# Optimization experiments

Hardware: AMD Instinct MI355X
Metric: run time of the kernel (lower is better)

The kernel has to match this reference:

```python
import jax, jax.numpy as jnp
import numpy as np

EPS = 1e-5  # torch LayerNorm default


def _ln(x, w, b):
    m = jnp.mean(x, axis=-1, keepdims=True)
    v = jnp.mean((x - m) ** 2, axis=-1, keepdims=True)
    return (x - m) / jnp.sqrt(v + EPS) * w + b


def _conv1x1(x, w, b):
    # x: [B,C,H,W], w: [O,C], b: [O]
    return jnp.einsum('bchw,oc->bohw', x, w) + b[None, :, None, None]


def setup_inputs() -> dict:
    key = jax.random.key(0)
    ks = jax.random.split(key, 5)
    B, Cin, H, W = 8, 384, 64, 64
    D, N = 128, 512
    s = lambda k, shape, scale=0.02: jax.random.normal(k, shape, jnp.float32) * scale
    return {
        'x': jax.random.normal(ks[0], (B, Cin, H, W), jnp.float32),
        'DR': jax.random.normal(ks[1], (N, D), jnp.float32),
        'conv_in_w': s(ks[2], (D, Cin)),
        'conv_in_b': jnp.zeros((D,), jnp.float32),
        'sem_w': s(ks[3], (D, D)),
        'sem_b': jnp.zeros((D,), jnp.float32),
        'norm1_w': jnp.ones((D,), jnp.float32),
        'norm1_b': jnp.zeros((D,), jnp.float32),
        'norm2_w': jnp.ones((D,), jnp.float32),
        'norm2_b': jnp.zeros((D,), jnp.float32),
        'conv_out_w': s(ks[4], (Cin, D)),
        'conv_out_b': jnp.zeros((Cin,), jnp.float32),
    }


def reference(x, DR, conv_in_w, conv_in_b, sem_w, sem_b, norm1_w, norm1_b,
              norm2_w, norm2_b, conv_out_w, conv_out_b):
    B, _, H, W = x.shape
    N = DR.shape[0]
    x_align = _conv1x1(x, conv_in_w, conv_in_b)                      # [B,D,H,W]
    x_sem = _conv1x1(x_align, sem_w, sem_b)                          # semantic_extra (1x1 conv)
    x_sem = x_sem.transpose(0, 2, 3, 1).reshape(B, H * W, -1)        # [B,HW,D]
    x_sem = _ln(x_sem, norm1_w, norm1_b)
    dr = _ln(DR, norm2_w, norm2_b).T                                 # [D,N] (same for all batches)
    # NOTE: original applies norm_1 TWICE for the numerator (faithful quirk)
    c_u = jnp.einsum('bld,dn->bln', _ln(x_sem, norm1_w, norm1_b), dr)  # [B,HW,N]
    c_d_l = jnp.sqrt(jnp.sum(x_sem ** 2, axis=-1, keepdims=True))      # [B,HW,1]
    c_d_r = jnp.sqrt(jnp.sum(dr ** 2, axis=0, keepdims=True))[None]    # [1,1,N]
    sim = c_u / (c_d_l * c_d_r)
    sim_soft = jax.nn.softmax(sim, axis=-1)                          # [B,HW,N]
    sim2d = sim_soft.transpose(0, 2, 1).reshape(B, N, H, W)
    degrad = jnp.einsum('bln,dn->bdl', sim_soft, dr).reshape(B, -1, H, W)  # [B,D,H,W]
    # pow-mask with per-batch min-max normalization
    mask_v = jnp.max(sim2d ** 3, axis=1, keepdims=True)              # [B,1,H,W]
    mn = jnp.min(mask_v.reshape(B, -1), axis=1).reshape(B, 1, 1, 1)
    mx = jnp.max(mask_v.reshape(B, -1), axis=1).reshape(B, 1, 1, 1)
    mask_v = 1.0 - (mask_v - mn) / (mx - mn)
    # topk row selection (torch fancy indexing gives [B,B,K,N]; squeeze(1) is a no-op for B>1)
    max_values = jnp.max(sim_soft, axis=2)                           # [B,HW]
    K = (H * W) // 50
    _, top_idx = jax.lax.top_k(max_values, K)                        # [B,K]
    results = jnp.take(sim_soft, top_idx, axis=1)                    # [B,B,K,N]
    out_img = _conv1x1(degrad, conv_out_w, conv_out_b)               # [B,Cin,H,W]
    return (mask_v, out_img, results)
```

## Files before the change

### kernel.cpp

```cpp
#include <hip/hip_runtime.h>
#include <cstdint>

#define EPS 1e-5f
#define BB   8
#define CIN  384
#define HWs  4096
#define LT   32768
#define DD   128
#define NN   512
#define TOPK 81
#define PSTR 528

typedef short short8 __attribute__((ext_vector_type(8)));
typedef float f32x4  __attribute__((ext_vector_type(4)));

__device__ __forceinline__ unsigned short f2bf(float x) {
  unsigned u = __float_as_uint(x);
  u += 0x7fffu + ((u >> 16) & 1u);
  return (unsigned short)(u >> 16);
}
__device__ __forceinline__ float bf2f(unsigned u16) {
  return __uint_as_float(u16 << 16);
}
__device__ __forceinline__ void put_frag(unsigned short* buf, int tile, int rc, int k, float v) {
  int ks = k >> 5, g = (k >> 3) & 3, j = k & 7;
  int basehw = ((tile * 4 + ks) * 2) * 512 + (g * 16 + rc) * 8 + j;
  unsigned short hi = f2bf(v);
  buf[basehw] = hi;
  buf[basehw + 512] = f2bf(v - bf2f(hi));
}

__device__ __forceinline__ void dr_body(int n, int lane, const float* __restrict__ DR,
    const float* __restrict__ w2, const float* __restrict__ b2,
    const float* __restrict__ w1, const float* __restrict__ b1,
    unsigned short* __restrict__ drwF, unsigned short* __restrict__ drlnF,
    float* __restrict__ t2, float* __restrict__ rcr) {
  const float* row = DR + n * DD;
  float x0 = row[lane], x1 = row[lane + 64];
  float s = x0 + x1, sq = x0 * x0 + x1 * x1;
  #pragma unroll
  for (int o = 32; o; o >>= 1) { s += __shfl_xor(s, o); sq += __shfl_xor(sq, o); }
  float m = s * (1.f / 128.f);
  float v = sq * (1.f / 128.f) - m * m;
  float inv = rsqrtf(v + EPS);
  float y0 = (x0 - m) * inv * w2[lane] + b2[lane];
  float y1 = (x1 - m) * inv * w2[lane + 64] + b2[lane + 64];
  int nt = n >> 4, cc = n & 15;
  put_frag(drwF, nt, cc, lane, y0 * w1[lane]);
  put_frag(drwF, nt, cc, lane + 64, y1 * w1[lane + 64]);
  int ks = n >> 5, gB = (n >> 3) & 3, j = n & 7;
  {
    int d = lane;
    unsigned short hi = f2bf(y0);
    int base = (((d >> 4) * 16 + ks) * 2) * 512 + (gB * 16 + (d & 15)) * 8 + j;
    drlnF[base] = hi;
    drlnF[base + 512] = f2bf(y0 - bf2f(hi));
  }
  {
    int d = lane + 64;
    unsigned short hi = f2bf(y1);
    int base = (((d >> 4) * 16 + ks) * 2) * 512 + (gB * 16 + (d & 15)) * 8 + j;
    drlnF[base] = hi;
    drlnF[base + 512] = f2bf(y1 - bf2f(hi));
  }
  float pt2 = y0 * b1[lane] + y1 * b1[lane + 64];
  float pss = y0 * y0 + y1 * y1;
  #pragma unroll
  for (int o = 32; o; o >>= 1) { pt2 += __shfl_xor(pt2, o); pss += __shfl_xor(pss, o); }
  if (lane == 0) { t2[n] = pt2; rcr[n] = rsqrtf(pss); }
}

__device__ __forceinline__ void bprep_body(const float* __restrict__ src,
    unsigned short* __restrict__ dst, int K, int rt, int kb, int t) {
  int m = t >> 4, kg = t & 15;
  int k0 = kb * 128 + kg * 8;
  const float* s = src + (size_t)(rt * 16 + m) * K + k0;
  float4 f0 = *(const float4*)s;
  float4 f1 = *(const float4*)(s + 4);
  float vs[8] = {f0.x, f0.y, f0.z, f0.w, f1.x, f1.y, f1.z, f1.w};
  short8 hi, lo;
  #pragma unroll
  for (int j = 0; j < 8; ++j) {
    unsigned short h = f2bf(vs[j]);
    hi[j] = (short)h;
    lo[j] = (short)f2bf(vs[j] - bf2f(h));
  }
  int nkt = K >> 5;
  int ks = k0 >> 5, g = (k0 >> 3) & 3;
  short8* D8 = (short8*)dst;
  int base = ((rt * nkt + ks) * 2) * 64 + g * 16 + m;
  D8[base] = hi;
  D8[base + 64] = lo;
}

__global__ __launch_bounds__(256) void k_prep(const float* __restrict__ DR,
    const float* __restrict__ n2w, const float* __restrict__ n2b,
    const float* __restrict__ n1w, const float* __restrict__ n1b,
    unsigned short* __restrict__ drwF, unsigned short* __restrict__ drlnF,
    float* __restrict__ t2, float* __restrict__ rcr,
    const float* __restrict__ win, unsigned short* __restrict__ WinF,
    const float* __restrict__ sw, unsigned short* __restrict__ semWF,
    const float* __restrict__ wout, unsigned short* __restrict__ WoF) {
  int blk = blockIdx.x, t = threadIdx.x;
  if (blk < 128) {
    dr_body(blk * 4 + (t >> 6), t & 63, DR, n2w, n2b, n1w, n1b, drwF, drlnF, t2, rcr);
  } else if (blk < 152) {
    int idx = blk - 128;
    bprep_body(win, WinF, CIN, idx & 7, idx >> 3, t);
  } else if (blk < 160) {
    bprep_body(sw, semWF, DD, blk - 152, 0, t);
  } else {
    bprep_body(wout, WoF, DD, blk - 160, 0, t);
  }
}

__global__ __launch_bounds__(256, 3) void k_convsem(const float* __restrict__ x,
    const unsigned short* __restrict__ WinF, const float* __restrict__ bin,
    const unsigned short* __restrict__ semWF, const float* __restrict__ sb,
    const float* __restrict__ w1, const float* __restrict__ b1,
    unsigned short* __restrict__ ApF, float* __restrict__ rclv) {
  __shared__ float xt[CIN * 33];
  __shared__ float sredS[32][4], sredQ[32][4];
  __shared__ float rowM[32], rowI[32];
  int t = threadIdx.x;
  int w = t >> 6, lane = t & 63, m = lane & 15, g = lane >> 4;
  int l0 = blockIdx.x * 32;
  int b = l0 >> 12, hw0 = l0 & 4095;
  {
    const float* xs = x + (size_t)b * CIN * HWs + (size_t)(t >> 3) * HWs + hw0 + (t & 7) * 4;
    float4 v[12];
    #pragma unroll
    for (int r = 0; r < 12; ++r)
      v[r] = *(const float4*)(xs + (size_t)(r * 32) * HWs);
    #pragma unroll
    for (int r = 0; r < 12; ++r) {
      float* d = &xt[(r * 32 + (t >> 3)) * 33 + (t & 7) * 4];
      d[0] = v[r].x; d[1] = v[r].y; d[2] = v[r].z; d[3] = v[r].w;
    }
  }
  __syncthreads();
  const short8* B8 = (const short8*)WinF;
  f32x4 acc[2][2];
  #pragma unroll
  for (int lt = 0; lt < 2; ++lt)
    #pragma unroll
    for (int j2 = 0; j2 < 2; ++j2) acc[lt][j2] = (f32x4){0.f, 0.f, 0.f, 0.f};
  for (int ks = 0; ks < 12; ++ks) {
    short8 ah[2], al[2];
    #pragma unroll
    for (int lt = 0; lt < 2; ++lt) {
      #pragma unroll
      for (int j = 0; j < 8; ++j) {
        float xv = xt[(ks * 32 + g * 8 + j) * 33 + lt * 16 + m];
        unsigned short h = f2bf(xv);
        ah[lt][j] = (short)h;
        al[lt][j] = (short)f2bf(xv - bf2f(h));
      }
    }
    #pragma unroll
    for (int j2 = 0; j2 < 2; ++j2) {
      int dt = w * 2 + j2;
      short8 bh = B8[((dt * 12 + ks) * 2 + 0) * 64 + lane];
      short8 bl = B8[((dt * 12 + ks) * 2 + 1) * 64 + lane];
      #pragma unroll
      for (int lt = 0; lt < 2; ++lt) {
        acc[lt][j2] = __builtin_amdgcn_mfma_f32_16x16x32_bf16(ah[lt], bh, acc[lt][j2], 0, 0, 0);
        acc[lt][j2] = __builtin_amdgcn_mfma_f32_16x16x32_bf16(ah[lt], bl, acc[lt][j2], 0, 0, 0);
        acc[lt][j2] = __builtin_amdgcn_mfma_f32_16x16x32_bf16(al[lt], bh, acc[lt][j2], 0, 0, 0);
      }
    }
  }
  __syncthreads();
  unsigned int* plane = (unsigned int*)xt;
  {
    float bia[2] = {bin[w * 32 + m], bin[w * 32 + 16 + m]};
    #pragma unroll
    for (int lt = 0; lt < 2; ++lt)
      #pragma unroll
      for (int j2 = 0; j2 < 2; ++j2)
        #pragma unroll
        for (int r = 0; r < 4; ++r) {
          float v = acc[lt][j2][r] + bia[j2];
          unsigned short h = f2bf(v);
          unsigned short lo = f2bf(v - bf2f(h));
          plane[(lt * 16 + g * 4 + r) * 132 + (w * 2 + j2) * 16 + m] =
              (unsigned)h | ((unsigned)lo << 16);
        }
  }
  __syncthreads();
  const short8* S8 = (const short8*)semWF;
  f32x4 acc2[2][2];
  #pragma unroll
  for (int lt = 0; lt < 2; ++lt)
    #pragma unroll
    for (int j2 = 0; j2 < 2; ++j2) acc2[lt][j2] = (f32x4){0.f, 0.f, 0.f, 0.f};
  #pragma unroll
  for (int ks2 = 0; ks2 < 4; ++ks2) {
    short8 ah2[2], al2[2];
    #pragma unroll
    for (int lt = 0; lt < 2; ++lt) {
      const unsigned* src = &plane[(lt * 16 + m) * 132 + ks2 * 32 + g * 8];
      uint4 p0 = *(const uint4*)(src);
      uint4 p1 = *(const uint4*)(src + 4);
      unsigned uu[8] = {p0.x, p0.y, p0.z, p0.w, p1.x, p1.y, p1.z, p1.w};
      unsigned* ahp = (unsigned*)&ah2[lt];
      unsigned* alp = (unsigned*)&al2[lt];
      #pragma unroll
      for (int jj = 0; jj < 4; ++jj) {
        unsigned e0 = uu[2 * jj], e1 = uu[2 * jj + 1];
        ahp[jj] = (e0 & 0xffffu) | (e1 << 16);
        alp[jj] = (e0 >> 16) | (e1 & 0xffff0000u);
      }
    }
    #pragma unroll
    for (int j2 = 0; j2 < 2; ++j2) {
      int dt = w * 2 + j2;
      short8 bh = S8[((dt * 4 + ks2) * 2 + 0) * 64 + lane];
      short8 bl = S8[((dt * 4 + ks2) * 2 + 1) * 64 + lane];
      #pragma unroll
      for (int lt = 0; lt < 2; ++lt) {
        acc2[lt][j2] = __builtin_amdgcn_mfma_f32_16x16x32_bf16(ah2[lt], bh, acc2[lt][j2], 0, 0, 0);
        acc2[lt][j2] = __builtin_amdgcn_mfma_f32_16x16x32_bf16(ah2[lt], bl, acc2[lt][j2], 0, 0, 0);
        acc2[lt][j2] = __builtin_amdgcn_mfma_f32_16x16x32_bf16(al2[lt], bh, acc2[lt][j2], 0, 0, 0);
      }
    }
  }
  {
    float bia2[2] = {sb[w * 32 + m], sb[w * 32 + 16 + m]};
    #pragma unroll
    for (int lt = 0; lt < 2; ++lt)
      #pragma unroll
      for (int j2 = 0; j2 < 2; ++j2)
        #pragma unroll
        for (int r = 0; r < 4; ++r) acc2[lt][j2][r] += bia2[j2];
  }
  float s1[2][4], q1[2][4];
  #pragma unroll
  for (int lt = 0; lt < 2; ++lt)
    #pragma unroll
    for (int r = 0; r < 4; ++r) {
      float a = acc2[lt][0][r], b2v = acc2[lt][1][r];
      s1[lt][r] = a + b2v;
      q1[lt][r] = a * a + b2v * b2v;
    }
  #pragma unroll
  for (int o = 1; o < 16; o <<= 1)
    #pragma unroll
    for (int lt = 0; lt < 2; ++lt)
      #pragma unroll
      for (int r = 0; r < 4; ++r) {
        s1[lt][r] += __shfl_xor(s1[lt][r], o);
        q1[lt][r] += __shfl_xor(q1[lt][r], o);
      }
  if (m == 0) {
    #pragma unroll
    for (int lt = 0; lt < 2; ++lt)
      #pragma unroll
      for (int r = 0; r < 4; ++r) {
        sredS[lt * 16 + g * 4 + r][w] = s1[lt][r];
        sredQ[lt * 16 + g * 4 + r][w] = q1[lt][r];
      }
  }
  __syncthreads();
  if (t < 32) {
    float S = sredS[t][0] + sredS[t][1] + sredS[t][2] + sredS[t][3];
    float Q = sredQ[t][0] + sredQ[t][1] + sredQ[t][2] + sredQ[t][3];
    float mu = S * (1.f / 128.f);
    float var = Q * (1.f / 128.f) - mu * mu;
    rowM[t] = mu;
    rowI[t] = rsqrtf(var + EPS);
  }
  __syncthreads();
  float w1v[2] = {w1[w * 32 + m], w1[w * 32 + 16 + m]};
  float b1v[2] = {b1[w * 32 + m], b1[w * 32 + 16 + m]};
  #pragma unroll
  for (int lt = 0; lt < 2; ++lt)
    #pragma unroll
    for (int r = 0; r < 4; ++r) {
      float mu = rowM[lt * 16 + g * 4 + r];
      float iv = rowI[lt * 16 + g * 4 + r];
      float y0 = (acc2[lt][0][r] - mu) * iv * w1v[0] + b1v[0];
      float y1 = (acc2[lt][1][r] - mu) * iv * w1v[1] + b1v[1];
      acc2[lt][0][r] = y0; acc2[lt][1][r] = y1;
      s1[lt][r] = y0 + y1;
      q1[lt][r] = y0 * y0 + y1 * y1;
    }
  #pragma unroll
  for (int o = 1; o < 16; o <<= 1)
    #pragma unroll
    for (int lt = 0; lt < 2; ++lt)
      #pragma unroll
      for (int r = 0; r < 4; ++r) {
        s1[lt][r] += __shfl_xor(s1[lt][r], o);
        q1[lt][r] += __shfl_xor(q1[lt][r], o);
      }
  if (m == 0) {
    #pragma unroll
    for (int lt = 0; lt < 2; ++lt)
      #pragma unroll
      for (int r = 0; r < 4; ++r) {
        sredS[lt * 16 + g * 4 + r][w] = s1[lt][r];
        sredQ[lt * 16 + g * 4 + r][w] = q1[lt][r];
      }
  }
  __syncthreads();
  if (t < 32) {
    float S = sredS[t][0] + sredS[t][1] + sredS[t][2] + sredS[t][3];
    float Q = sredQ[t][0] + sredQ[t][1] + sredQ[t][2] + sredQ[t][3];
    float m2 = S * (1.f / 128.f);
    float v2 = Q * (1.f / 128.f) - m2 * m2;
    float inv2 = rsqrtf(v2 + EPS);
    float rcl = rsqrtf(Q);
    rowM[t] = m2;
    rowI[t] = inv2 * rcl;
    rclv[l0 + t] = rcl;
  }
  __syncthreads();
  float* planef = (float*)xt;
  #pragma unroll
  for (int lt = 0; lt < 2; ++lt)
    #pragma unroll
    for (int r = 0; r < 4; ++r) {
      float m2 = rowM[lt * 16 + g * 4 + r];
      float sc = rowI[lt * 16 + g * 4 + r];
      planef[(lt * 16 + g * 4 + r) * 132 + w * 32 + m] = (acc2[lt][0][r] - m2) * sc;
      planef[(lt * 16 + g * 4 + r) * 132 + w * 32 + 16 + m] = (acc2[lt][1][r] - m2) * sc;
    }
  __syncthreads();
  short8* O8 = (short8*)ApF;
  #pragma unroll
  for (int it = 0; it < 2; ++it) {
    int idx = it * 256 + t;
    int l = idx & 31, dq = idx >> 5;
    const float* src = &planef[l * 132 + dq * 8];
    float4 f0 = *(const float4*)src;
    float4 f1 = *(const float4*)(src + 4);
    float vs[8] = {f0.x, f0.y, f0.z, f0.w, f1.x, f1.y, f1.z, f1.w};
    short8 hi, lo;
    #pragma unroll
    for (int j = 0; j < 8; ++j) {
      unsigned short h = f2bf(vs[j]);
      hi[j] = (short)h;
      lo[j] = (short)f2bf(vs[j] - bf2f(h));
    }
    int ltg = (l0 + l) >> 4;
    int idx8 = ((ltg * 4 + (dq >> 2)) * 2) * 64 + (dq & 3) * 16 + (l & 15);
    O8[idx8] = hi;
    O8[idx8 + 64] = lo;
  }
}

__global__ __launch_bounds__(256, 4) void k_sdeg(const unsigned short* __restrict__ ApF,
    const unsigned short* __restrict__ drwF, const float* __restrict__ t2g,
    const float* __restrict__ rcrg, const float* __restrict__ rclg,
    const unsigned short* __restrict__ drlnF, const unsigned short* __restrict__ WoF,
    const float* __restrict__ bo,
    unsigned short* __restrict__ pF, float* __restrict__ maxv,
    float* __restrict__ out_img) {
  __shared__ __align__(16) float sredM[32][4];
  __shared__ __align__(16) float sredS[32][4];
  __shared__ __align__(16) unsigned short plds[32 * PSTR];
  int t = threadIdx.x;
  int w = t >> 6, lane = t & 63, c = lane & 15, g = lane >> 4;
  int l0 = blockIdx.x * 32;
  int lt0 = blockIdx.x * 2;
  const short8* A8 = (const short8*)ApF;
  const short8* B8 = (const short8*)drwF;
  f32x4 acc[2][8];
  #pragma unroll
  for (int il = 0; il < 2; ++il)
    #pragma unroll
    for (int jn = 0; jn < 8; ++jn) acc[il][jn] = (f32x4){0.f, 0.f, 0.f, 0.f};
  #pragma unroll
  for (int ks = 0; ks < 4; ++ks) {
    short8 ah0 = A8[((lt0 * 4 + ks) * 2 + 0) * 64 + lane];
    short8 al0 = A8[((lt0 * 4 + ks) * 2 + 1) * 64 + lane];
    short8 ah1 = A8[(((lt0 + 1) * 4 + ks) * 2 + 0) * 64 + lane];
    short8 al1 = A8[(((lt0 + 1) * 4 + ks) * 2 + 1) * 64 + lane];
    #pragma unroll
    for (int jn = 0; jn < 8; ++jn) {
      int nt = w * 8 + jn;
      short8 bh = B8[((nt * 4 + ks) * 2 + 0) * 64 + lane];
      short8 bl = B8[((nt * 4 + ks) * 2 + 1) * 64 + lane];
      acc[0][jn] = __builtin_amdgcn_mfma_f32_16x16x32_bf16(ah0, bh, acc[0][jn], 0, 0, 0);
      acc[0][jn] = __builtin_amdgcn_mfma_f32_16x16x32_bf16(ah0, bl, acc[0][jn], 0, 0, 0);
      acc[0][jn] = __builtin_amdgcn_mfma_f32_16x16x32_bf16(al0, bh, acc[0][jn], 0, 0, 0);
      acc[1][jn] = __builtin_amdgcn_mfma_f32_16x16x32_bf16(ah1, bh, acc[1][jn], 0, 0, 0);
      acc[1][jn] = __builtin_amdgcn_mfma_f32_16x16x32_bf16(ah1, bl, acc[1][jn], 0, 0, 0);
      acc[1][jn] = __builtin_amdgcn_mfma_f32_16x16x32_bf16(al1, bh, acc[1][jn], 0, 0, 0);
    }
  }
  float rcrv[8], t2v[8];
  #pragma unroll
  for (int jn = 0; jn < 8; ++jn) {
    int n = w * 128 + jn * 16 + c;
    rcrv[jn] = rcrg[n]; t2v[jn] = t2g[n];
  }
  float rclr[2][4];
  #pragma unroll
  for (int il = 0; il < 2; ++il)
    #pragma unroll
    for (int r = 0; r < 4; ++r)
      rclr[il][r] = rclg[l0 + il * 16 + g * 4 + r];
  float M[2][4];
  #pragma unroll
  for (int il = 0; il < 2; ++il)
    #pragma unroll
    for (int r = 0; r < 4; ++r) M[il][r] = -1e30f;
  #pragma unroll
  for (int il = 0; il < 2; ++il)
    #pragma unroll
    for (int jn = 0; jn < 8; ++jn) {
      f32x4 a = acc[il][jn];
      #pragma unroll
      for (int r = 0; r < 4; ++r) {
        float s = rcrv[jn] * (a[r] + rclr[il][r] * t2v[jn]);
        a[r] = s;
        M[il][r] = fmaxf(M[il][r], s);
      }
      acc[il][jn] = a;
    }
  #pragma unroll
  for (int o = 1; o < 16; o <<= 1)
    #pragma unroll
    for (int il = 0; il < 2; ++il)
      #pragma unroll
      for (int r = 0; r < 4; ++r)
        M[il][r] = fmaxf(M[il][r], __shfl_xor(M[il][r], o));
  if (c == 0) {
    #pragma unroll
    for (int il = 0; il < 2; ++il)
      #pragma unroll
      for (int r = 0; r < 4; ++r)
        sredM[il * 16 + g * 4 + r][w] = M[il][r];
  }
  __syncthreads();
  float Mf[2][4];
  #pragma unroll
  for (int il = 0; il < 2; ++il)
    #pragma unroll
    for (int r = 0; r < 4; ++r) {
      f32x4 mv = *(const f32x4*)(&sredM[il * 16 + g * 4 + r][0]);
      Mf[il][r] = fmaxf(fmaxf(mv[0], mv[1]), fmaxf(mv[2], mv[3]));
    }
  float S[2][4];
  #pragma unroll
  for (int il = 0; il < 2; ++il)
    #pragma unroll
    for (int r = 0; r < 4; ++r) S[il][r] = 0.f;
  #pragma unroll
  for (int il = 0; il < 2; ++il)
    #pragma unroll
    for (int jn = 0; jn < 8; ++jn) {
      f32x4 a = acc[il][jn];
      #pragma unroll
      for (int r = 0; r < 4; ++r) {
        float e = __expf(a[r] - Mf[il][r]);
        a[r] = e;
        S[il][r] += e;
      }
      acc[il][jn] = a;
    }
  #pragma unroll
  for (int o = 1; o < 16; o <<= 1)
    #pragma unroll
    for (int il = 0; il < 2; ++il)
      #pragma unroll
      for (int r = 0; r < 4; ++r)
        S[il][r] += __shfl_xor(S[il][r], o);
  if (c == 0) {
    #pragma unroll
    for (int il = 0; il < 2; ++il)
      #pragma unroll
      for (int r = 0; r < 4; ++r)
        sredS[il * 16 + g * 4 + r][w] = S[il][r];
  }
  __syncthreads();
  float RS[2][4];
  #pragma unroll
  for (int il = 0; il < 2; ++il)
    #pragma unroll
    for (int r = 0; r < 4; ++r) {
      f32x4 sv = *(const f32x4*)(&sredS[il * 16 + g * 4 + r][0]);
      float tot = sv[0] + sv[1] + sv[2] + sv[3];
      RS[il][r] = 1.f / tot;
    }
  if (w == 0 && c == 0) {
    #pragma unroll
    for (int il = 0; il < 2; ++il)
      #pragma unroll
      for (int r = 0; r < 4; ++r)
        maxv[l0 + il * 16 + g * 4 + r] = RS[il][r];
  }
  #pragma unroll
  for (int il = 0; il < 2; ++il)
    #pragma unroll
    for (int jn = 0; jn < 8; ++jn)
      #pragma unroll
      for (int r = 0; r < 4; ++r)
        plds[(il * 16 + g * 4 + r) * PSTR + w * 128 + jn * 16 + c] =
            f2bf(acc[il][jn][r] * RS[il][r]);
  __syncthreads();
  const short8* D8 = (const short8*)drlnF;
  f32x4 accd[2][2];
  #pragma unroll
  for (int lt = 0; lt < 2; ++lt)
    #pragma unroll
    for (int j2 = 0; j2 < 2; ++j2) accd[lt][j2] = (f32x4){0.f, 0.f, 0.f, 0.f};
  for (int ks = 0; ks < 16; ++ks) {
    const unsigned short* sp = &plds[c * PSTR + ks * 32 + g * 8];
    short8 pa0 = *(const short8*)sp;
    short8 pa1 = *(const short8*)(sp + 16 * PSTR);
    #pragma unroll
    for (int j2 = 0; j2 < 2; ++j2) {
      int dt = w * 2 + j2;
      short8 bh = D8[((dt * 16 + ks) * 2 + 0) * 64 + lane];
      short8 bl = D8[((dt * 16 + ks) * 2 + 1) * 64 + lane];
      accd[0][j2] = __builtin_amdgcn_mfma_f32_16x16x32_bf16(pa0, bh, accd[0][j2], 0, 0, 0);
      accd[0][j2] = __builtin_amdgcn_mfma_f32_16x16x32_bf16(pa0, bl, accd[0][j2], 0, 0, 0);
      accd[1][j2] = __builtin_amdgcn_mfma_f32_16x16x32_bf16(pa1, bh, accd[1][j2], 0, 0, 0);
      accd[1][j2] = __builtin_amdgcn_mfma_f32_16x16x32_bf16(pa1, bl, accd[1][j2], 0, 0, 0);
    }
  }
  short8* P8o = (short8*)pF;
  #pragma unroll
  for (int it = 0; it < 8; ++it) {
    int slot = it * 256 + t;
    int ltl = slot >> 10;
    int ks = (slot >> 6) & 15;
    int gB = (slot >> 4) & 3;
    int mrow = slot & 15;
    int row = ltl * 16 + mrow;
    int n0 = ks * 32 + gB * 8;
    short8 v = *(const short8*)(&plds[row * PSTR + n0]);
    __builtin_nontemporal_store(v, &P8o[blockIdx.x * 2048 + slot]);
  }
  __syncthreads();
  float* smem2 = (float*)plds;
  #pragma unroll
  for (int lt = 0; lt < 2; ++lt)
    #pragma unroll
    for (int j2 = 0; j2 < 2; ++j2)
      #pragma unroll
      for (int r = 0; r < 4; ++r)
        smem2[(lt * 16 + g * 4 + r) * 132 + w * 32 + j2 * 16 + c] = accd[lt][j2][r];
  __syncthreads();
  const short8* W8 = (const short8*)WoF;
  f32x4 acco[2][6];
  #pragma unroll
  for (int lt = 0; lt < 2; ++lt)
    #pragma unroll
    for (int ot = 0; ot < 6; ++ot) acco[lt][ot] = (f32x4){0.f, 0.f, 0.f, 0.f};
  #pragma unroll
  for (int ks2 = 0; ks2 < 4; ++ks2) {
    short8 dh[2];
    #pragma unroll
    for (int lt = 0; lt < 2; ++lt) {
      const float* src = &smem2[(lt * 16 + c) * 132 + ks2 * 32 + g * 8];
      float4 f0 = *(const float4*)src;
      float4 f1 = *(const float4*)(src + 4);
      float vs[8] = {f0.x, f0.y, f0.z, f0.w, f1.x, f1.y, f1.z, f1.w};
      #pragma unroll
      for (int j = 0; j < 8; ++j) dh[lt][j] = (short)f2bf(vs[j]);
    }
    #pragma unroll
    for (int ot = 0; ot < 6; ++ot) {
      int otg = w * 6 + ot;
      short8 wh = W8[((otg * 4 + ks2) * 2 + 0) * 64 + lane];
      short8 wl = W8[((otg * 4 + ks2) * 2 + 1) * 64 + lane];
      #pragma unroll
      for (int lt = 0; lt < 2; ++lt) {
        acco[lt][ot] = __builtin_amdgcn_mfma_f32_16x16x32_bf16(dh[lt], wh, acco[lt][ot], 0, 0, 0);
        acco[lt][ot] = __builtin_amdgcn_mfma_f32_16x16x32_bf16(dh[lt], wl, acco[lt][ot], 0, 0, 0);
      }
    }
  }
  int b = l0 >> 12, hw0 = l0 & 4095;
  float* ob = out_img + (size_t)b * CIN * HWs + hw0;
  #pragma unroll
  for (int ot = 0; ot < 6; ++ot) {
    float bov = bo[w * 96 + ot * 16 + c];
    #pragma unroll
    for (int lt = 0; lt < 2; ++lt) {
      f32x4 vv = acco[lt][ot];
      f32x4 o4 = {vv[0] + bov, vv[1] + bov, vv[2] + bov, vv[3] + bov};
      __builtin_nontemporal_store(o4,
          (f32x4*)(ob + (size_t)(w * 96 + ot * 16 + c) * HWs + lt * 16 + g * 4));
    }
  }
}

__global__ __launch_bounds__(256) void k_topk(const float* __restrict__ maxv,
                                              int* __restrict__ tix,
                                              float* __restrict__ outm) {
  __shared__ unsigned int hist[4][256];
  __shared__ unsigned long long slist[TOPK];
  __shared__ unsigned long long bc_prefix;
  __shared__ int bc_need, scount;
  __shared__ float smn[4], smx[4];
  int b = blockIdx.x, t = threadIdx.x;
  int w = t >> 6;
  unsigned long long key[16];
  #pragma unroll
  for (int j = 0; j < 16; ++j) {
    int idx = t + j * 256;
    unsigned int bits = __float_as_uint(maxv[b * HWs + idx]);
    key[j] = ((unsigned long long)bits << 12) | (unsigned)(4095 - idx);
  }
  {
    float c3[16];
    float mn = 1e30f, mx = -1e30f;
    #pragma unroll
    for (int j = 0; j < 16; ++j) {
      float x = __uint_as_float((unsigned)(key[j] >> 12));
      float cc = x * x * x;
      c3[j] = cc;
      mn = fminf(mn, cc); mx = fmaxf(mx, cc);
    }
    #pragma unroll
    for (int o = 32; o; o >>= 1) { mn = fminf(mn, __shfl_xor(mn, o)); mx = fmaxf(mx, __shfl_xor(mx, o)); }
    if ((t & 63) == 0) { smn[w] = mn; smx[w] = mx; }
    __syncthreads();
    mn = fminf(fminf(smn[0], smn[1]), fminf(smn[2], smn[3]));
    mx = fmaxf(fmaxf(smx[0], smx[1]), fmaxf(smx[2], smx[3]));
    float sc = 1.f / (mx - mn);
    #pragma unroll
    for (int j = 0; j < 16; ++j)
      outm[b * HWs + t + j * 256] = 1.f - (c3[j] - mn) * sc;
  }
  if (t == 0) { bc_prefix = 0ull; bc_need = TOPK; scount = 0; }
  for (int r = 0; r < 6; ++r) {
    int shift = 40 - 8 * r;
    unsigned int* hflat = (unsigned int*)hist;
    hflat[t] = 0; hflat[t + 256] = 0; hflat[t + 512] = 0; hflat[t + 768] = 0;
    __syncthreads();
    unsigned long long prefix = bc_prefix;
    int bins[16];
    #pragma unroll
    for (int j = 0; j < 16; ++j)
      bins[j] = ((key[j] >> (shift + 8)) == prefix) ? (int)((key[j] >> shift) & 255) : -1;
    #pragma unroll
    for (int j = 0; j < 16; ++j) {
      if (bins[j] >= 0) {
        int cnt = 1;
        #pragma unroll
        for (int j2 = j + 1; j2 < 16; ++j2)
          if (bins[j2] == bins[j]) { bins[j2] = -1; ++cnt; }
        atomicAdd(&hist[w][bins[j]], (unsigned)cnt);
      }
    }
    __syncthreads();
    if (t < 64) {
      int cb[4], s = 0;
      #pragma unroll
      for (int j = 0; j < 4; ++j) {
        int bin = 255 - (t * 4 + j);
        cb[j] = (int)(hist[0][bin] + hist[1][bin] + hist[2][bin] + hist[3][bin]);
        s += cb[j];
      }
      int P = s;
      #pragma unroll
      for (int o = 1; o < 64; o <<= 1) {
        int u = __shfl_up(P, o);
        if (t >= o) P += u;
      }
      int need = bc_need;
      unsigned long long mask = __ballot(P >= need);
      int first = __ffsll((long long)mask) - 1;
      if (t == first) {
        int acc = P - s;
        #pragma unroll
        for (int j = 0; j < 4; ++j) {
          if (acc + cb[j] >= need) {
            bc_prefix = (prefix << 8) | (unsigned)(255 - (t * 4 + j));
            bc_need = need - acc;
            break;
          }
          acc += cb[j];
        }
      }
    }
    __syncthreads();
  }
  unsigned long long K81 = bc_prefix;
  #pragma unroll
  for (int j = 0; j < 16; ++j)
    if (key[j] >= K81) {
      int pos = atomicAdd(&scount, 1);
      slist[pos] = key[j];
    }
  __syncthreads();
  if (t < TOPK) {
    unsigned long long mine = slist[t];
    int rank = 0;
    for (int i = 0; i < TOPK; ++i) rank += (slist[i] > mine) ? 1 : 0;
    tix[b * TOPK + rank] = 4095 - (int)(mine & 0xFFFull);
  }
}

__global__ __launch_bounds__(128) void k_gather(const unsigned short* __restrict__ pF,
    const int* __restrict__ tix, float* __restrict__ outr) {
  int gB_ = blockIdx.x;
  int k = gB_ % TOPK;
  int bb = gB_ / TOPK;
  int b2 = bb & 7, b = bb >> 3;
  int l = b * HWs + tix[b2 * TOPK + k];
  int lt = l >> 4, mrow = l & 15;
  int t = threadIdx.x;
  int ks = t >> 3, gq = (t >> 1) & 3, j0 = (t & 1) * 4;
  int base = ((lt * 16 + ks) * 64 + gq * 16 + mrow) * 8 + j0;
  const unsigned* src = (const unsigned*)(pF + base);
  unsigned u0 = src[0], u1 = src[1];
  f32x4 v = {bf2f(u0 & 0xffffu), bf2f(u0 >> 16), bf2f(u1 & 0xffffu), bf2f(u1 >> 16)};
  __builtin_nontemporal_store(v, (f32x4*)(outr + (size_t)gB_ * NN + t * 4));
}

extern "C" void kernel_launch(void* const* d_in, const int* in_sizes, int n_in,
                              void* d_out, int out_size, void* d_ws, size_t ws_size,
                              hipStream_t stream) {
  const float* x    = (const float*)d_in[0];
  const float* DR   = (const float*)d_in[1];
  const float* win  = (const float*)d_in[2];
  const float* bin  = (const float*)d_in[3];
  const float* sw   = (const float*)d_in[4];
  const float* sb   = (const float*)d_in[5];
  const float* n1w  = (const float*)d_in[6];
  const float* n1b  = (const float*)d_in[7];
  const float* n2w  = (const float*)d_in[8];
  const float* n2b  = (const float*)d_in[9];
  const float* wout = (const float*)d_in[10];
  const float* bout = (const float*)d_in[11];
  float* out = (float*)d_out;
  float* W = (float*)d_ws;

  unsigned short* drwF  = (unsigned short*)(W);
  float* t2   = W + 65536;
  float* rcr  = W + 66048;
  float* rclv = W + 66560;
  float* maxv = W + 99328;
  unsigned short* drlnF = (unsigned short*)(W + 132096);
  unsigned short* WoF   = (unsigned short*)(W + 197632);
  unsigned short* WinF  = (unsigned short*)(W + 246784);
  unsigned short* semWF = (unsigned short*)(W + 295936);
  unsigned short* ApF   = (unsigned short*)(W + 312320);
  unsigned short* pF    = (unsigned short*)(W + 4506624);
  int*   tix  = (int*)(W + 12895232);

  float* out_mask = out;
  float* out_img  = out + 32768;
  float* out_res  = out + 32768 + 12582912;

  k_prep   <<<184, 256, 0, stream>>>(DR, n2w, n2b, n1w, n1b, drwF, drlnF, t2, rcr,
                                     win, WinF, sw, semWF, wout, WoF);
  k_convsem<<<1024, 256, 0, stream>>>(x, WinF, bin, semWF, sb, n1w, n1b, ApF, rclv);
  k_sdeg   <<<1024, 256, 0, stream>>>(ApF, drwF, t2, rcr, rclv, drlnF, WoF, bout,
                                      pF, maxv, out_img);
  k_topk   <<<BB,   256, 0, stream>>>(maxv, tix, out_mask);
  k_gather <<<BB * BB * TOPK, 128, 0, stream>>>(pF, tix, out_res);
}
```

Before: 218.4 us.

## Recompute selected softmax rows in gather instead of materializing full probability matrix

```diff
diff --git a/kernel.cpp b/kernel.cpp
--- a/kernel.cpp
+++ b/kernel.cpp
@@ -355,7 +355,7 @@
     const float* __restrict__ rcrg, const float* __restrict__ rclg,
     const unsigned short* __restrict__ drlnF, const unsigned short* __restrict__ WoF,
     const float* __restrict__ bo,
-    unsigned short* __restrict__ pF, float* __restrict__ maxv,
+    float* __restrict__ mfv, float* __restrict__ maxv,
     float* __restrict__ out_img) {
   __shared__ __align__(16) float sredM[32][4];
   __shared__ __align__(16) float sredS[32][4];
@@ -489,8 +489,10 @@
     #pragma unroll
     for (int il = 0; il < 2; ++il)
       #pragma unroll
-      for (int r = 0; r < 4; ++r)
+      for (int r = 0; r < 4; ++r) {
         maxv[l0 + il * 16 + g * 4 + r] = RS[il][r];
+        mfv[l0 + il * 16 + g * 4 + r] = Mf[il][r];
+      }
   }
   #pragma unroll
   for (int il = 0; il < 2; ++il)
@@ -522,19 +524,6 @@
       accd[1][j2] = __builtin_amdgcn_mfma_f32_16x16x32_bf16(pa1, bl, accd[1][j2], 0, 0, 0);
     }
   }
-  short8* P8o = (short8*)pF;
-  #pragma unroll
-  for (int it = 0; it < 8; ++it) {
-    int slot = it * 256 + t;
-    int ltl = slot >> 10;
-    int ks = (slot >> 6) & 15;
-    int gB = (slot >> 4) & 3;
-    int mrow = slot & 15;
-    int row = ltl * 16 + mrow;
-    int n0 = ks * 32 + gB * 8;
-    short8 v = *(const short8*)(&plds[row * PSTR + n0]);
-    __builtin_nontemporal_store(v, &P8o[blockIdx.x * 2048 + slot]);
-  }
   __syncthreads();
   float* smem2 = (float*)plds;
   #pragma unroll
@@ -583,9 +572,8 @@
     #pragma unroll
     for (int lt = 0; lt < 2; ++lt) {
       f32x4 vv = acco[lt][ot];
-      f32x4 o4 = {vv[0] + bov, vv[1] + bov, vv[2] + bov, vv[3] + bov};
-      __builtin_nontemporal_store(o4,
-          (f32x4*)(ob + (size_t)(w * 96 + ot * 16 + c) * HWs + lt * 16 + g * 4));
+      float4 o4 = {vv[0] + bov, vv[1] + bov, vv[2] + bov, vv[3] + bov};
+      *(float4*)(ob + (size_t)(w * 96 + ot * 16 + c) * HWs + lt * 16 + g * 4) = o4;
     }
   }
 }
@@ -698,21 +686,71 @@
   }
 }
 
-__global__ __launch_bounds__(128) void k_gather(const unsigned short* __restrict__ pF,
+__global__ __launch_bounds__(256) void k_gather(const unsigned short* __restrict__ ApF,
+    const unsigned short* __restrict__ drwF, const float* __restrict__ t2g,
+    const float* __restrict__ rcrg, const float* __restrict__ rclg,
+    const float* __restrict__ mfv, const float* __restrict__ rsv,
     const int* __restrict__ tix, float* __restrict__ outr) {
-  int gB_ = blockIdx.x;
-  int k = gB_ % TOPK;
-  int bb = gB_ / TOPK;
-  int b2 = bb & 7, b = bb >> 3;
-  int l = b * HWs + tix[b2 * TOPK + k];
-  int lt = l >> 4, mrow = l & 15;
+  __shared__ float As[8][128];
+  __shared__ float rclS[8], mfS[8], rsS[8];
+  int blk = blockIdx.x;
+  int k = blk % TOPK, b2 = blk / TOPK;
+  int lloc = tix[b2 * TOPK + k];
   int t = threadIdx.x;
-  int ks = t >> 3, gq = (t >> 1) & 3, j0 = (t & 1) * 4;
-  int base = ((lt * 16 + ks) * 64 + gq * 16 + mrow) * 8 + j0;
-  const unsigned* src = (const unsigned*)(pF + base);
-  unsigned u0 = src[0], u1 = src[1];
-  f32x4 v = {bf2f(u0 & 0xffffu), bf2f(u0 >> 16), bf2f(u1 & 0xffffu), bf2f(u1 >> 16)};
-  __builtin_nontemporal_store(v, (f32x4*)(outr + (size_t)gB_ * NN + t * 4));
+  {
+    int idx = t;
+    #pragma unroll
+    for (int it = 0; it < 4; ++it, idx += 256) {
+      int bb = idx >> 7, d = idx & 127;
+      int grow = bb * HWs + lloc;
+      int ltg = grow >> 4, mrow = grow & 15;
+      int ks = d >> 5, gq = (d >> 3) & 3, j = d & 7;
+      int sbase = (((ltg * 4 + ks) * 2) * 64 + gq * 16 + mrow) * 8 + j;
+      As[bb][d] = bf2f(ApF[sbase]) + bf2f(ApF[sbase + 512]);
+    }
+    if (t < 8) {
+      int grow = t * HWs + lloc;
+      rclS[t] = rclg[grow];
+      mfS[t] = mfv[grow];
+      rsS[t] = rsv[grow];
+    }
+  }
+  __syncthreads();
+  #pragma unroll
+  for (int half = 0; half < 2; ++half) {
+    int n = half * 256 + t;
+    int nt = n >> 4, cc = n & 15;
+    float dot[8];
+    #pragma unroll
+    for (int bb = 0; bb < 8; ++bb) dot[bb] = 0.f;
+    #pragma unroll
+    for (int d8 = 0; d8 < 16; ++d8) {
+      int ks = d8 >> 2, gq = d8 & 3;
+      int sbase = ((nt * 4 + ks) * 2) * 512 + (gq * 16 + cc) * 8;
+      const unsigned* hp = (const unsigned*)(drwF + sbase);
+      const unsigned* lp = (const unsigned*)(drwF + sbase + 512);
+      float bcol[8];
+      #pragma unroll
+      for (int jj = 0; jj < 4; ++jj) {
+        unsigned h2 = hp[jj], l2 = lp[jj];
+        bcol[2 * jj]     = bf2f(h2 & 0xffffu) + bf2f(l2 & 0xffffu);
+        bcol[2 * jj + 1] = bf2f(h2 >> 16)     + bf2f(l2 >> 16);
+      }
+      #pragma unroll
+      for (int bb = 0; bb < 8; ++bb) {
+        #pragma unroll
+        for (int j = 0; j < 8; ++j)
+          dot[bb] += As[bb][d8 * 8 + j] * bcol[j];
+      }
+    }
+    float rcr = rcrg[n], t2 = t2g[n];
+    #pragma unroll
+    for (int bb = 0; bb < 8; ++bb) {
+      float s = rcr * (dot[bb] + rclS[bb] * t2);
+      float p = __expf(s - mfS[bb]) * rsS[bb];
+      outr[((size_t)(bb * 8 + b2) * TOPK + k) * NN + n] = p;
+    }
+  }
 }
 
 extern "C" void kernel_launch(void* const* d_in, const int* in_sizes, int n_in,
@@ -743,7 +781,7 @@
   unsigned short* WinF  = (unsigned short*)(W + 246784);
   unsigned short* semWF = (unsigned short*)(W + 295936);
   unsigned short* ApF   = (unsigned short*)(W + 312320);
-  unsigned short* pF    = (unsigned short*)(W + 4506624);
+  float* mfv  = W + 4506624;
   int*   tix  = (int*)(W + 12895232);
 
   float* out_mask = out;
@@ -754,7 +792,8 @@
                                      win, WinF, sw, semWF, wout, WoF);
   k_convsem<<<1024, 256, 0, stream>>>(x, WinF, bin, semWF, sb, n1w, n1b, ApF, rclv);
   k_sdeg   <<<1024, 256, 0, stream>>>(ApF, drwF, t2, rcr, rclv, drlnF, WoF, bout,
-                                      pF, maxv, out_img);
+                                      mfv, maxv, out_img);
   k_topk   <<<BB,   256, 0, stream>>>(maxv, tix, out_mask);
-  k_gather <<<BB * BB * TOPK, 128, 0, stream>>>(pF, tix, out_res);
-}
+  k_gather <<<BB * TOPK, 256, 0, stream>>>(ApF, drwF, t2, rcr, rclv, mfv, maxv,
+                                           tix, out_res);
+}
```

Result: slower. 234.7 us (+7.5%).
